# Kernel tuning notes

Measured on AMD Instinct MI355X. Metric: run time of the kernel, lower is better.

Reference implementation:

```python
import jax, jax.numpy as jnp
import numpy as np

B, T, C, H = 2, 2048, 2048, 16
HD = C // H  # head_dim = 128


def setup_inputs() -> dict:
    key = jax.random.key(0)
    k1, k2, k3 = jax.random.split(key, 3)
    x = jax.random.normal(k1, (B, T, C), dtype=jnp.float32)
    # causal mask: positions with mask==0 are blocked (masked_fill(mask==0, -inf))
    mask = jnp.tril(jnp.ones((T, T), dtype=bool))[None, None]  # [1,1,T,T]
    W_qkv = jax.random.normal(k2, (C, 3 * C), dtype=jnp.float32) * (C ** -0.5)
    W_proj = jax.random.normal(k3, (C, C), dtype=jnp.float32) * (C ** -0.5)
    b_proj = jnp.zeros((C,), dtype=jnp.float32)
    return {"x": x, "mask": mask, "W_qkv": W_qkv, "W_proj": W_proj, "b_proj": b_proj}


def reference(x, mask, W_qkv, W_proj, b_proj):
    # QKV projection (Linear, bias=False)
    qkv = jnp.einsum('btc,cd->btd', x, W_qkv)            # [B,T,3C]
    qkv = qkv.reshape(B, T, 3, H, HD)
    q = qkv[:, :, 0].transpose(0, 2, 1, 3)               # [B,H,T,HD]
    k = qkv[:, :, 1].transpose(0, 2, 1, 3)
    v = qkv[:, :, 2].transpose(0, 2, 1, 3)
    # scaled dot-product attention (dropout is identity in eval)
    att = jnp.einsum('bhqd,bhkd->bhqk', q, k) / jnp.sqrt(jnp.float32(HD))
    att = jnp.where(mask, att, -jnp.inf)
    att = jax.nn.softmax(att, axis=-1)
    y = jnp.einsum('bhqk,bhkd->bhqd', att, v)            # [B,H,T,HD]
    y = y.transpose(0, 2, 1, 3).reshape(B, T, C)
    return jnp.einsum('btc,cd->btd', y, W_proj) + b_proj
```

## Files before the change

kernel.cpp:

```cpp
#include <hip/hip_runtime.h>
#include <hip/hip_bf16.h>

#define B_  2
#define T_  2048
#define C_  2048
#define H_  16
#define HD_ 128

using bf16x8 = __attribute__((ext_vector_type(8))) __bf16;
using f32x4  = __attribute__((ext_vector_type(4))) float;

__device__ __forceinline__ unsigned short f2bs(float f) {
    __hip_bfloat16 h = __float2bfloat16(f);
    return __builtin_bit_cast(unsigned short, h);
}

__device__ __forceinline__ void gload_lds16(const unsigned short* g, unsigned short* l) {
    __builtin_amdgcn_global_load_lds(
        (const __attribute__((address_space(1))) unsigned int*)g,
        (__attribute__((address_space(3))) unsigned int*)l, 16, 0, 0);
}

__global__ __launch_bounds__(256) void k_prep(const float* __restrict__ x,
                                              unsigned short* __restrict__ XB,
                                              const float* __restrict__ Wqkv,
                                              unsigned short* __restrict__ WQKVT,
                                              const float* __restrict__ Wproj,
                                              unsigned short* __restrict__ WPROJT) {
    __shared__ unsigned short t[64][65];
    int blk = blockIdx.x;
    int tid = threadIdx.x;
    if (blk < 8192) {
        int i = blk * 256 + tid;
        float4 v = reinterpret_cast<const float4*>(x)[i];
        ushort4 o;
        o.x = f2bs(v.x); o.y = f2bs(v.y); o.z = f2bs(v.z); o.w = f2bs(v.w);
        reinterpret_cast<ushort4*>(XB)[i] = o;
        return;
    }
    const float* in;
    unsigned short* out;
    int K = 2048, N, bx, by;
    if (blk < 11264) {
        in = Wqkv; out = WQKVT; N = 6144;
        bx = (blk - 8192) % 96; by = (blk - 8192) / 96;
    } else {
        in = Wproj; out = WPROJT; N = 2048;
        bx = (blk - 11264) % 32; by = (blk - 11264) / 32;
    }
    int k0 = by * 64, n0 = bx * 64;
#pragma unroll
    for (int p = 0; p < 4; ++p) {
        int idx = p * 256 + tid;
        int r = idx >> 4, c = (idx & 15) << 2;
        float4 v = *reinterpret_cast<const float4*>(in + (long)(k0 + r) * N + n0 + c);
        t[r][c] = f2bs(v.x); t[r][c + 1] = f2bs(v.y);
        t[r][c + 2] = f2bs(v.z); t[r][c + 3] = f2bs(v.w);
    }
    __syncthreads();
#pragma unroll
    for (int p = 0; p < 4; ++p) {
        int idx = p * 256 + tid;
        int r = idx >> 4, c = (idx & 15) << 2;
        ushort4 o;
        o.x = t[c][r]; o.y = t[c + 1][r]; o.z = t[c + 2][r]; o.w = t[c + 3][r];
        *reinterpret_cast<ushort4*>(out + (long)(n0 + r) * K + k0 + c) = o;
    }
}

template <int MODE>
__global__ __launch_bounds__(256, 2) void k_gemm(const unsigned short* __restrict__ A,
                                                 const unsigned short* __restrict__ Bt,
                                                 int M, int N, int K,
                                                 unsigned short* __restrict__ qkv,
                                                 float* __restrict__ out,
                                                 const float* __restrict__ bias) {
    __shared__ __align__(16) unsigned short lA[2][128 * 32];
    __shared__ __align__(16) unsigned short lB[2][128 * 32];

    int tid = threadIdx.x;
    int wave = tid >> 6, lane = tid & 63;
    int quad = lane >> 4, l16 = lane & 15;
    int wr = (wave >> 1) * 64, wc = (wave & 1) * 64;
    int m0 = blockIdx.y * 128, n0 = blockIdx.x * 128;

    int lrow = lane >> 2;
    int lcol = (lane & 3) << 3;
    const unsigned short* gA0 = A + (long)(m0 + wave * 32 + lrow) * K + lcol;
    const unsigned short* gA1 = A + (long)(m0 + wave * 32 + 16 + lrow) * K + lcol;
    const unsigned short* gB0 = Bt + (long)(n0 + wave * 32 + lrow) * K + lcol;
    const unsigned short* gB1 = Bt + (long)(n0 + wave * 32 + 16 + lrow) * K + lcol;
    int lofs0 = wave * 1024, lofs1 = wave * 1024 + 512;

    f32x4 zero = {0.f, 0.f, 0.f, 0.f};
    f32x4 acc[4][4];
#pragma unroll
    for (int i = 0; i < 4; ++i)
#pragma unroll
        for (int j = 0; j < 4; ++j) acc[i][j] = zero;

    for (int k0 = 0; k0 < K; k0 += 64) {
        __syncthreads();
#pragma unroll
        for (int h = 0; h < 2; ++h) {
            int kk = k0 + h * 32;
            gload_lds16(gA0 + kk, &lA[h][lofs0]);
            gload_lds16(gA1 + kk, &lA[h][lofs1]);
            gload_lds16(gB0 + kk, &lB[h][lofs0]);
            gload_lds16(gB1 + kk, &lB[h][lofs1]);
        }
        __syncthreads();
#pragma unroll
        for (int h = 0; h < 2; ++h) {
            bf16x8 af[4], bfr[4];
#pragma unroll
            for (int i = 0; i < 4; ++i)
                af[i] = *reinterpret_cast<const bf16x8*>(&lA[h][(wr + i * 16 + l16) * 32 + quad * 8]);
#pragma unroll
            for (int j = 0; j < 4; ++j)
                bfr[j] = *reinterpret_cast<const bf16x8*>(&lB[h][(wc + j * 16 + l16) * 32 + quad * 8]);
#pragma unroll
            for (int i = 0; i < 4; ++i)
#pragma unroll
                for (int j = 0; j < 4; ++j)
                    acc[i][j] = __builtin_amdgcn_mfma_f32_16x16x32_bf16(af[i], bfr[j], acc[i][j], 0, 0, 0);
        }
    }

#pragma unroll
    for (int i = 0; i < 4; ++i) {
#pragma unroll
        for (int j = 0; j < 4; ++j) {
#pragma unroll
            for (int r = 0; r < 4; ++r) {
                int m = m0 + wr + i * 16 + quad * 4 + r;
                int n = n0 + wc + j * 16 + l16;
                float v = acc[i][j][r];
                if (MODE == 0) {
                    int s = n >> 11, col = n & 2047;
                    int h = col >> 7, hd = col & 127;
                    int b = m >> 11, t = m & 2047;
                    long base = (long)s * (B_ * H_ * T_ * HD_);
                    if (s == 2)
                        qkv[base + ((long)(b * H_ + h) * HD_ + hd) * T_ + t] = f2bs(v);
                    else
                        qkv[base + ((long)(b * H_ + h) * T_ + t) * HD_ + hd] = f2bs(v);
                } else {
                    out[(long)m * N + n] = v + bias[n];
                }
            }
        }
    }
}

__global__ __launch_bounds__(256, 3) void k_attn(const unsigned short* __restrict__ qkv,
                                                 unsigned short* __restrict__ y) {
    __shared__ __align__(16) unsigned short lK[64 * 136];
    __shared__ __align__(16) unsigned short lVt[128 * 72];
    __shared__ __align__(16) unsigned short lP[4][16 * 72];

    int tid = threadIdx.x;
    int wave = tid >> 6, lane = tid & 63;
    int quad = lane >> 4, l16 = lane & 15;
    int bh = blockIdx.x;
    int qb = ((int)gridDim.y - 1 - (int)blockIdx.y) * 64;

    const unsigned short* Qh = qkv + (long)bh * (T_ * HD_);
    const unsigned short* Kh = qkv + (long)(B_ * H_) * T_ * HD_ + (long)bh * (T_ * HD_);
    const unsigned short* Vt = qkv + 2L * (B_ * H_) * T_ * HD_ + (long)bh * (HD_ * T_);

    bf16x8 aQ[4];
    int qrow = qb + wave * 16 + l16;
#pragma unroll
    for (int kk = 0; kk < 4; ++kk)
        aQ[kk] = *reinterpret_cast<const bf16x8*>(Qh + (long)qrow * HD_ + kk * 32 + quad * 8);

    const int kR0 = tid >> 4,           kC = (tid & 15) << 3;
    const int vR0 = tid >> 3,           vC = (tid & 7) << 3;

    int4 kr0, kr1, kr2, kr3, vr0, vr1, vr2, vr3;
    {
        long ko = 0;
        kr0 = *reinterpret_cast<const int4*>(Kh + (ko + kR0)      * HD_ + kC);
        kr1 = *reinterpret_cast<const int4*>(Kh + (ko + kR0 + 16) * HD_ + kC);
        kr2 = *reinterpret_cast<const int4*>(Kh + (ko + kR0 + 32) * HD_ + kC);
        kr3 = *reinterpret_cast<const int4*>(Kh + (ko + kR0 + 48) * HD_ + kC);
        vr0 = *reinterpret_cast<const int4*>(Vt + (long)(vR0)      * T_ + ko + vC);
        vr1 = *reinterpret_cast<const int4*>(Vt + (long)(vR0 + 32) * T_ + ko + vC);
        vr2 = *reinterpret_cast<const int4*>(Vt + (long)(vR0 + 64) * T_ + ko + vC);
        vr3 = *reinterpret_cast<const int4*>(Vt + (long)(vR0 + 96) * T_ + ko + vC);
    }

    float m_l = -1e30f, l_l = 0.f;
    f32x4 O[8];
    f32x4 zero = {0.f, 0.f, 0.f, 0.f};
#pragma unroll
    for (int h = 0; h < 8; ++h) O[h] = zero;

    const int q_abs = qb + wave * 16 + l16;
    const float scl = 0.08838834764831845f;
    const int kbend = qb + 64;

    for (int kb = 0; kb < kbend; kb += 64) {
        __syncthreads();

        *reinterpret_cast<int4*>(&lK[(kR0)      * 136 + kC]) = kr0;
        *reinterpret_cast<int4*>(&lK[(kR0 + 16) * 136 + kC]) = kr1;
        *reinterpret_cast<int4*>(&lK[(kR0 + 32) * 136 + kC]) = kr2;
        *reinterpret_cast<int4*>(&lK[(kR0 + 48) * 136 + kC]) = kr3;
        *reinterpret_cast<int4*>(&lVt[(vR0)      * 72 + vC]) = vr0;
        *reinterpret_cast<int4*>(&lVt[(vR0 + 32) * 72 + vC]) = vr1;
        *reinterpret_cast<int4*>(&lVt[(vR0 + 64) * 72 + vC]) = vr2;
        *reinterpret_cast<int4*>(&lVt[(vR0 + 96) * 72 + vC]) = vr3;

        __syncthreads();

        {
            int nkb = kb + 64;
            long ko = (nkb < kbend) ? nkb : 0;
            kr0 = *reinterpret_cast<const int4*>(Kh + (ko + kR0)      * HD_ + kC);
            kr1 = *reinterpret_cast<const int4*>(Kh + (ko + kR0 + 16) * HD_ + kC);
            kr2 = *reinterpret_cast<const int4*>(Kh + (ko + kR0 + 32) * HD_ + kC);
            kr3 = *reinterpret_cast<const int4*>(Kh + (ko + kR0 + 48) * HD_ + kC);
            vr0 = *reinterpret_cast<const int4*>(Vt + (long)(vR0)      * T_ + ko + vC);
            vr1 = *reinterpret_cast<const int4*>(Vt + (long)(vR0 + 32) * T_ + ko + vC);
            vr2 = *reinterpret_cast<const int4*>(Vt + (long)(vR0 + 64) * T_ + ko + vC);
            vr3 = *reinterpret_cast<const int4*>(Vt + (long)(vR0 + 96) * T_ + ko + vC);
        }

        f32x4 s[4];
#pragma unroll
        for (int st = 0; st < 4; ++st) s[st] = zero;
#pragma unroll
        for (int kk = 0; kk < 4; ++kk) {
#pragma unroll
            for (int st = 0; st < 4; ++st) {
                bf16x8 kf = *reinterpret_cast<const bf16x8*>(
                    &lK[(st * 16 + l16) * 136 + kk * 32 + quad * 8]);
                s[st] = __builtin_amdgcn_mfma_f32_16x16x32_bf16(kf, aQ[kk], s[st], 0, 0, 0);
            }
        }

        float xv[4][4];
        float mx = -1e30f;
#pragma unroll
        for (int st = 0; st < 4; ++st)
#pragma unroll
            for (int r = 0; r < 4; ++r) {
                int key = kb + st * 16 + quad * 4 + r;
                float v = (key <= q_abs) ? s[st][r] * scl : -1e30f;
                xv[st][r] = v;
                mx = fmaxf(mx, v);
            }
        mx = fmaxf(mx, __shfl_xor(mx, 16));
        mx = fmaxf(mx, __shfl_xor(mx, 32));
        float mn = fmaxf(m_l, mx);
        float al = __expf(m_l - mn);
        float rs = 0.f;
#pragma unroll
        for (int st = 0; st < 4; ++st)
#pragma unroll
            for (int r = 0; r < 4; ++r) {
                float e = __expf(xv[st][r] - mn);
                xv[st][r] = e;
                rs += e;
            }
        rs += __shfl_xor(rs, 16);
        rs += __shfl_xor(rs, 32);
        m_l = mn;
        l_l = l_l * al + rs;

#pragma unroll
        for (int st = 0; st < 4; ++st) {
            ushort4 pk;
            pk.x = f2bs(xv[st][0]); pk.y = f2bs(xv[st][1]);
            pk.z = f2bs(xv[st][2]); pk.w = f2bs(xv[st][3]);
            *reinterpret_cast<ushort4*>(&lP[wave][l16 * 72 + st * 16 + quad * 4]) = pk;
        }

        float alr[4];
#pragma unroll
        for (int r = 0; r < 4; ++r) alr[r] = __shfl(al, quad * 4 + r);
#pragma unroll
        for (int h = 0; h < 8; ++h)
#pragma unroll
            for (int r = 0; r < 4; ++r) O[h][r] *= alr[r];

#pragma unroll
        for (int kc = 0; kc < 2; ++kc) {
            bf16x8 pf = *reinterpret_cast<const bf16x8*>(
                &lP[wave][l16 * 72 + kc * 32 + quad * 8]);
#pragma unroll
            for (int h = 0; h < 8; ++h) {
                bf16x8 vf = *reinterpret_cast<const bf16x8*>(
                    &lVt[(h * 16 + l16) * 72 + kc * 32 + quad * 8]);
                O[h] = __builtin_amdgcn_mfma_f32_16x16x32_bf16(pf, vf, O[h], 0, 0, 0);
            }
        }
    }

    int b = bh >> 4, hh = bh & 15;
#pragma unroll
    for (int r = 0; r < 4; ++r) {
        int t = qb + wave * 16 + quad * 4 + r;
        float inv = 1.f / __shfl(l_l, quad * 4 + r);
#pragma unroll
        for (int h = 0; h < 8; ++h)
            y[(long)(b * T_ + t) * C_ + hh * HD_ + h * 16 + l16] = f2bs(O[h][r] * inv);
    }
}

extern "C" void kernel_launch(void* const* d_in, const int* in_sizes, int n_in,
                              void* d_out, int out_size, void* d_ws, size_t ws_size,
                              hipStream_t stream) {
    const float* x     = (const float*)d_in[0];
    const float* Wqkv  = (const float*)d_in[2];
    const float* Wproj = (const float*)d_in[3];
    const float* bproj = (const float*)d_in[4];
    float* out = (float*)d_out;

    unsigned short* XB     = (unsigned short*)d_ws;
    unsigned short* WQKVT  = XB + 8388608;
    unsigned short* WPROJT = WQKVT + 12582912;
    unsigned short* QKV    = WPROJT + 4194304;
    if (ws_size < 100663296) return;

    k_prep<<<12288, 256, 0, stream>>>(x, XB, Wqkv, WQKVT, Wproj, WPROJT);
    k_gemm<0><<<dim3(6144 / 128, 4096 / 128), 256, 0, stream>>>(XB, WQKVT, 4096, 6144, 2048,
                                                                QKV, nullptr, nullptr);
    k_attn<<<dim3(32, 32), 256, 0, stream>>>(QKV, XB);
    k_gemm<1><<<dim3(2048 / 128, 4096 / 128), 256, 0, stream>>>(XB, WPROJT, 4096, 2048, 2048,
                                                                nullptr, out, bproj);
}
```

Before: 388.8 us.

## Double-buffer GEMM LDS tiles and raise wave priority around attention MFMAs

```diff
diff --git a/kernel.cpp b/kernel.cpp
--- a/kernel.cpp
+++ b/kernel.cpp
@@ -75,8 +75,8 @@
                                                  unsigned short* __restrict__ qkv,
                                                  float* __restrict__ out,
                                                  const float* __restrict__ bias) {
-    __shared__ __align__(16) unsigned short lA[2][128 * 32];
-    __shared__ __align__(16) unsigned short lB[2][128 * 32];
+    __shared__ __align__(16) unsigned short lA[2][2][128 * 32];
+    __shared__ __align__(16) unsigned short lB[2][2][128 * 32];
 
     int tid = threadIdx.x;
     int wave = tid >> 6, lane = tid & 63;
@@ -99,33 +99,47 @@
 #pragma unroll
         for (int j = 0; j < 4; ++j) acc[i][j] = zero;
 
-    for (int k0 = 0; k0 < K; k0 += 64) {
-        __syncthreads();
+    auto stage = [&](int bi, int k0) {
 #pragma unroll
         for (int h = 0; h < 2; ++h) {
             int kk = k0 + h * 32;
-            gload_lds16(gA0 + kk, &lA[h][lofs0]);
-            gload_lds16(gA1 + kk, &lA[h][lofs1]);
-            gload_lds16(gB0 + kk, &lB[h][lofs0]);
-            gload_lds16(gB1 + kk, &lB[h][lofs1]);
-        }
-        __syncthreads();
+            gload_lds16(gA0 + kk, &lA[bi][h][lofs0]);
+            gload_lds16(gA1 + kk, &lA[bi][h][lofs1]);
+            gload_lds16(gB0 + kk, &lB[bi][h][lofs0]);
+            gload_lds16(gB1 + kk, &lB[bi][h][lofs1]);
+        }
+    };
+    auto compute = [&](int bi) {
 #pragma unroll
         for (int h = 0; h < 2; ++h) {
             bf16x8 af[4], bfr[4];
 #pragma unroll
             for (int i = 0; i < 4; ++i)
-                af[i] = *reinterpret_cast<const bf16x8*>(&lA[h][(wr + i * 16 + l16) * 32 + quad * 8]);
+                af[i] = *reinterpret_cast<const bf16x8*>(
+                    &lA[bi][h][(wr + i * 16 + l16) * 32 + quad * 8]);
 #pragma unroll
             for (int j = 0; j < 4; ++j)
-                bfr[j] = *reinterpret_cast<const bf16x8*>(&lB[h][(wc + j * 16 + l16) * 32 + quad * 8]);
+                bfr[j] = *reinterpret_cast<const bf16x8*>(
+                    &lB[bi][h][(wc + j * 16 + l16) * 32 + quad * 8]);
 #pragma unroll
             for (int i = 0; i < 4; ++i)
 #pragma unroll
                 for (int j = 0; j < 4; ++j)
-                    acc[i][j] = __builtin_amdgcn_mfma_f32_16x16x32_bf16(af[i], bfr[j], acc[i][j], 0, 0, 0);
-        }
-    }
+                    acc[i][j] = __builtin_amdgcn_mfma_f32_16x16x32_bf16(af[i], bfr[j],
+                                                                        acc[i][j], 0, 0, 0);
+        }
+    };
+
+    stage(0, 0);
+    __syncthreads();
+    int cur = 0;
+    for (int k0 = 64; k0 < K; k0 += 64) {
+        stage(cur ^ 1, k0);
+        compute(cur);
+        __syncthreads();
+        cur ^= 1;
+    }
+    compute(cur);
 
 #pragma unroll
     for (int i = 0; i < 4; ++i) {
@@ -231,6 +245,7 @@
         f32x4 s[4];
 #pragma unroll
         for (int st = 0; st < 4; ++st) s[st] = zero;
+        __builtin_amdgcn_s_setprio(1);
 #pragma unroll
         for (int kk = 0; kk < 4; ++kk) {
 #pragma unroll
@@ -240,6 +255,7 @@
                 s[st] = __builtin_amdgcn_mfma_f32_16x16x32_bf16(kf, aQ[kk], s[st], 0, 0, 0);
             }
         }
+        __builtin_amdgcn_s_setprio(0);
 
         float xv[4][4];
         float mx = -1e30f;
@@ -286,6 +302,7 @@
 #pragma unroll
             for (int r = 0; r < 4; ++r) O[h][r] *= alr[r];
 
+        __builtin_amdgcn_s_setprio(1);
 #pragma unroll
         for (int kc = 0; kc < 2; ++kc) {
             bf16x8 pf = *reinterpret_cast<const bf16x8*>(
@@ -297,6 +314,7 @@
                 O[h] = __builtin_amdgcn_mfma_f32_16x16x32_bf16(pf, vf, O[h], 0, 0, 0);
             }
         }
+        __builtin_amdgcn_s_setprio(0);
     }
 
     int b = bh >> 4, hh = bh & 15;
```

Result: slower. 427.9 us (+10.1%).

## Process two 16-row query tiles per wave in attention to reuse K/V fragments

Applied to the files above, without the earlier changes.

```diff
diff --git a/kernel.cpp b/kernel.cpp
--- a/kernel.cpp
+++ b/kernel.cpp
@@ -153,30 +153,33 @@
     }
 }
 
-__global__ __launch_bounds__(256, 3) void k_attn(const unsigned short* __restrict__ qkv,
+__global__ __launch_bounds__(256, 2) void k_attn(const unsigned short* __restrict__ qkv,
                                                  unsigned short* __restrict__ y) {
     __shared__ __align__(16) unsigned short lK[64 * 136];
     __shared__ __align__(16) unsigned short lVt[128 * 72];
-    __shared__ __align__(16) unsigned short lP[4][16 * 72];
+    __shared__ __align__(16) unsigned short lP[4][2][16 * 72];
 
     int tid = threadIdx.x;
     int wave = tid >> 6, lane = tid & 63;
     int quad = lane >> 4, l16 = lane & 15;
     int bh = blockIdx.x;
-    int qb = ((int)gridDim.y - 1 - (int)blockIdx.y) * 64;
+    int qb = ((int)gridDim.y - 1 - (int)blockIdx.y) * 128;
 
     const unsigned short* Qh = qkv + (long)bh * (T_ * HD_);
     const unsigned short* Kh = qkv + (long)(B_ * H_) * T_ * HD_ + (long)bh * (T_ * HD_);
     const unsigned short* Vt = qkv + 2L * (B_ * H_) * T_ * HD_ + (long)bh * (HD_ * T_);
 
-    bf16x8 aQ[4];
-    int qrow = qb + wave * 16 + l16;
-#pragma unroll
-    for (int kk = 0; kk < 4; ++kk)
-        aQ[kk] = *reinterpret_cast<const bf16x8*>(Qh + (long)qrow * HD_ + kk * 32 + quad * 8);
-
-    const int kR0 = tid >> 4,           kC = (tid & 15) << 3;
-    const int vR0 = tid >> 3,           vC = (tid & 7) << 3;
+    bf16x8 aQ0[4], aQ1[4];
+    const int q0_abs = qb + wave * 32 + l16;
+    const int q1_abs = q0_abs + 16;
+#pragma unroll
+    for (int kk = 0; kk < 4; ++kk) {
+        aQ0[kk] = *reinterpret_cast<const bf16x8*>(Qh + (long)q0_abs * HD_ + kk * 32 + quad * 8);
+        aQ1[kk] = *reinterpret_cast<const bf16x8*>(Qh + (long)q1_abs * HD_ + kk * 32 + quad * 8);
+    }
+
+    const int kR0 = tid >> 4, kC = (tid & 15) << 3;
+    const int vR0 = tid >> 3, vC = (tid & 7) << 3;
 
     int4 kr0, kr1, kr2, kr3, vr0, vr1, vr2, vr3;
     {
@@ -191,15 +194,15 @@
         vr3 = *reinterpret_cast<const int4*>(Vt + (long)(vR0 + 96) * T_ + ko + vC);
     }
 
-    float m_l = -1e30f, l_l = 0.f;
-    f32x4 O[8];
+    float m0_ = -1e30f, l0_ = 0.f, m1_ = -1e30f, l1_ = 0.f;
+    f32x4 O0[8], O1[8];
     f32x4 zero = {0.f, 0.f, 0.f, 0.f};
 #pragma unroll
-    for (int h = 0; h < 8; ++h) O[h] = zero;
-
-    const int q_abs = qb + wave * 16 + l16;
+    for (int h = 0; h < 8; ++h) { O0[h] = zero; O1[h] = zero; }
+
     const float scl = 0.08838834764831845f;
-    const int kbend = qb + 64;
+    const int kbend = qb + 128;
+    const int qmaxw = qb + wave * 32 + 31;
 
     for (int kb = 0; kb < kbend; kb += 64) {
         __syncthreads();
@@ -228,85 +231,144 @@
             vr3 = *reinterpret_cast<const int4*>(Vt + (long)(vR0 + 96) * T_ + ko + vC);
         }
 
-        f32x4 s[4];
-#pragma unroll
-        for (int st = 0; st < 4; ++st) s[st] = zero;
+        if (kb > qmaxw) continue;
+
+        f32x4 s0[4], s1[4];
+#pragma unroll
+        for (int st = 0; st < 4; ++st) { s0[st] = zero; s1[st] = zero; }
+        __builtin_amdgcn_s_setprio(1);
 #pragma unroll
         for (int kk = 0; kk < 4; ++kk) {
 #pragma unroll
             for (int st = 0; st < 4; ++st) {
                 bf16x8 kf = *reinterpret_cast<const bf16x8*>(
                     &lK[(st * 16 + l16) * 136 + kk * 32 + quad * 8]);
-                s[st] = __builtin_amdgcn_mfma_f32_16x16x32_bf16(kf, aQ[kk], s[st], 0, 0, 0);
-            }
-        }
-
-        float xv[4][4];
-        float mx = -1e30f;
-#pragma unroll
-        for (int st = 0; st < 4; ++st)
-#pragma unroll
-            for (int r = 0; r < 4; ++r) {
-                int key = kb + st * 16 + quad * 4 + r;
-                float v = (key <= q_abs) ? s[st][r] * scl : -1e30f;
-                xv[st][r] = v;
-                mx = fmaxf(mx, v);
-            }
-        mx = fmaxf(mx, __shfl_xor(mx, 16));
-        mx = fmaxf(mx, __shfl_xor(mx, 32));
-        float mn = fmaxf(m_l, mx);
-        float al = __expf(m_l - mn);
-        float rs = 0.f;
-#pragma unroll
-        for (int st = 0; st < 4; ++st)
-#pragma unroll
-            for (int r = 0; r < 4; ++r) {
-                float e = __expf(xv[st][r] - mn);
-                xv[st][r] = e;
-                rs += e;
-            }
-        rs += __shfl_xor(rs, 16);
-        rs += __shfl_xor(rs, 32);
-        m_l = mn;
-        l_l = l_l * al + rs;
-
-#pragma unroll
-        for (int st = 0; st < 4; ++st) {
-            ushort4 pk;
-            pk.x = f2bs(xv[st][0]); pk.y = f2bs(xv[st][1]);
-            pk.z = f2bs(xv[st][2]); pk.w = f2bs(xv[st][3]);
-            *reinterpret_cast<ushort4*>(&lP[wave][l16 * 72 + st * 16 + quad * 4]) = pk;
-        }
-
-        float alr[4];
-#pragma unroll
-        for (int r = 0; r < 4; ++r) alr[r] = __shfl(al, quad * 4 + r);
-#pragma unroll
-        for (int h = 0; h < 8; ++h)
-#pragma unroll
-            for (int r = 0; r < 4; ++r) O[h][r] *= alr[r];
-
+                s0[st] = __builtin_amdgcn_mfma_f32_16x16x32_bf16(kf, aQ0[kk], s0[st], 0, 0, 0);
+                s1[st] = __builtin_amdgcn_mfma_f32_16x16x32_bf16(kf, aQ1[kk], s1[st], 0, 0, 0);
+            }
+        }
+        __builtin_amdgcn_s_setprio(0);
+
+        {
+            float xv[4][4];
+            float mx = -1e30f;
+#pragma unroll
+            for (int st = 0; st < 4; ++st)
+#pragma unroll
+                for (int r = 0; r < 4; ++r) {
+                    int key = kb + st * 16 + quad * 4 + r;
+                    float v = (key <= q0_abs) ? s0[st][r] * scl : -1e30f;
+                    xv[st][r] = v;
+                    mx = fmaxf(mx, v);
+                }
+            mx = fmaxf(mx, __shfl_xor(mx, 16));
+            mx = fmaxf(mx, __shfl_xor(mx, 32));
+            float mn = fmaxf(m0_, mx);
+            float al = __expf(m0_ - mn);
+            float rs = 0.f;
+#pragma unroll
+            for (int st = 0; st < 4; ++st)
+#pragma unroll
+                for (int r = 0; r < 4; ++r) {
+                    float e = __expf(xv[st][r] - mn);
+                    xv[st][r] = e;
+                    rs += e;
+                }
+            rs += __shfl_xor(rs, 16);
+            rs += __shfl_xor(rs, 32);
+            m0_ = mn;
+            l0_ = l0_ * al + rs;
+#pragma unroll
+            for (int st = 0; st < 4; ++st) {
+                ushort4 pk;
+                pk.x = f2bs(xv[st][0]); pk.y = f2bs(xv[st][1]);
+                pk.z = f2bs(xv[st][2]); pk.w = f2bs(xv[st][3]);
+                *reinterpret_cast<ushort4*>(&lP[wave][0][l16 * 72 + st * 16 + quad * 4]) = pk;
+            }
+            float alr[4];
+#pragma unroll
+            for (int r = 0; r < 4; ++r) alr[r] = __shfl(al, quad * 4 + r);
+#pragma unroll
+            for (int h = 0; h < 8; ++h)
+#pragma unroll
+                for (int r = 0; r < 4; ++r) O0[h][r] *= alr[r];
+        }
+        {
+            float xv[4][4];
+            float mx = -1e30f;
+#pragma unroll
+            for (int st = 0; st < 4; ++st)
+#pragma unroll
+                for (int r = 0; r < 4; ++r) {
+                    int key = kb + st * 16 + quad * 4 + r;
+                    float v = (key <= q1_abs) ? s1[st][r] * scl : -1e30f;
+                    xv[st][r] = v;
+                    mx = fmaxf(mx, v);
+                }
+            mx = fmaxf(mx, __shfl_xor(mx, 16));
+            mx = fmaxf(mx, __shfl_xor(mx, 32));
+            float mn = fmaxf(m1_, mx);
+            float al = __expf(m1_ - mn);
+            float rs = 0.f;
+#pragma unroll
+            for (int st = 0; st < 4; ++st)
+#pragma unroll
+                for (int r = 0; r < 4; ++r) {
+                    float e = __expf(xv[st][r] - mn);
+                    xv[st][r] = e;
+                    rs += e;
+                }
+            rs += __shfl_xor(rs, 16);
+            rs += __shfl_xor(rs, 32);
+            m1_ = mn;
+            l1_ = l1_ * al + rs;
+#pragma unroll
+            for (int st = 0; st < 4; ++st) {
+                ushort4 pk;
+                pk.x = f2bs(xv[st][0]); pk.y = f2bs(xv[st][1]);
+                pk.z = f2bs(xv[st][2]); pk.w = f2bs(xv[st][3]);
+                *reinterpret_cast<ushort4*>(&lP[wave][1][l16 * 72 + st * 16 + quad * 4]) = pk;
+            }
+            float alr[4];
+#pragma unroll
+            for (int r = 0; r < 4; ++r) alr[r] = __shfl(al, quad * 4 + r);
+#pragma unroll
+            for (int h = 0; h < 8; ++h)
+#pragma unroll
+                for (int r = 0; r < 4; ++r) O1[h][r] *= alr[r];
+        }
+
+        __builtin_amdgcn_s_setprio(1);
 #pragma unroll
         for (int kc = 0; kc < 2; ++kc) {
-            bf16x8 pf = *reinterpret_cast<const bf16x8*>(
-                &lP[wave][l16 * 72 + kc * 32 + quad * 8]);
+            bf16x8 pf0 = *reinterpret_cast<const bf16x8*>(
+                &lP[wave][0][l16 * 72 + kc * 32 + quad * 8]);
+            bf16x8 pf1 = *reinterpret_cast<const bf16x8*>(
+                &lP[wave][1][l16 * 72 + kc * 32 + quad * 8]);
 #pragma unroll
             for (int h = 0; h < 8; ++h) {
                 bf16x8 vf = *reinterpret_cast<const bf16x8*>(
                     &lVt[(h * 16 + l16) * 72 + kc * 32 + quad * 8]);
-                O[h] = __builtin_amdgcn_mfma_f32_16x16x32_bf16(pf, vf, O[h], 0, 0, 0);
-            }
-        }
+                O0[h] = __builtin_amdgcn_mfma_f32_16x16x32_bf16(pf0, vf, O0[h], 0, 0, 0);
+                O1[h] = __builtin_amdgcn_mfma_f32_16x16x32_bf16(pf1, vf, O1[h], 0, 0, 0);
+            }
+        }
+        __builtin_amdgcn_s_setprio(0);
     }
 
     int b = bh >> 4, hh = bh & 15;
 #pragma unroll
     for (int r = 0; r < 4; ++r) {
-        int t = qb + wave * 16 + quad * 4 + r;
-        float inv = 1.f / __shfl(l_l, quad * 4 + r);
+        int t0 = qb + wave * 32 + quad * 4 + r;
+        float inv0 = 1.f / __shfl(l0_, quad * 4 + r);
 #pragma unroll
         for (int h = 0; h < 8; ++h)
-            y[(long)(b * T_ + t) * C_ + hh * HD_ + h * 16 + l16] = f2bs(O[h][r] * inv);
+            y[(long)(b * T_ + t0) * C_ + hh * HD_ + h * 16 + l16] = f2bs(O0[h][r] * inv0);
+        int t1 = t0 + 16;
+        float inv1 = 1.f / __shfl(l1_, quad * 4 + r);
+#pragma unroll
+        for (int h = 0; h < 8; ++h)
+            y[(long)(b * T_ + t1) * C_ + hh * HD_ + h * 16 + l16] = f2bs(O1[h][r] * inv1);
     }
 }
 
@@ -328,7 +390,7 @@
     k_prep<<<12288, 256, 0, stream>>>(x, XB, Wqkv, WQKVT, Wproj, WPROJT);
     k_gemm<0><<<dim3(6144 / 128, 4096 / 128), 256, 0, stream>>>(XB, WQKVT, 4096, 6144, 2048,
                                                                 QKV, nullptr, nullptr);
-    k_attn<<<dim3(32, 32), 256, 0, stream>>>(QKV, XB);
+    k_attn<<<dim3(32, 16), 256, 0, stream>>>(QKV, XB);
     k_gemm<1><<<dim3(2048 / 128, 4096 / 128), 256, 0, stream>>>(XB, WPROJT, 4096, 2048, 2048,
                                                                 nullptr, out, bproj);
 }
```

Result: slower. 408.6 us (+5.1%).
